# Kernel tuning notes

Measured on AMD Instinct MI355X. Metric: run time of the kernel, lower is better.

The kernel has to match this reference:

```python
import jax, jax.numpy as jnp
import numpy as np

D_MODEL = 1024
N_HEADS = 16
HEAD_DIM = D_MODEL // N_HEADS  # 64
WINDOW = 15
NUM_RANDOM = 2
B, L = 2, 2048


def setup_inputs() -> dict:
    key = jax.random.key(0)
    ks = jax.random.split(key, 5)
    x = jax.random.normal(ks[0], (B, L, D_MODEL), dtype=jnp.float32)
    # rotary angles: theta[t, j] = t / 10000^(2j/head_dim), shape [1, L, head_dim//2]
    inv_freq = 1.0 / (10000.0 ** (jnp.arange(0, HEAD_DIM, 2, dtype=jnp.float32) / HEAD_DIM))
    t = jnp.arange(L, dtype=jnp.float32)
    freqs = (t[:, None] * inv_freq[None, :])[None].astype(jnp.float32)  # [1,L,32]
    scale = 0.02
    wq = jax.random.normal(ks[1], (D_MODEL, D_MODEL), dtype=jnp.float32) * scale
    wk = jax.random.normal(ks[2], (D_MODEL, D_MODEL), dtype=jnp.float32) * scale
    wv = jax.random.normal(ks[3], (D_MODEL, D_MODEL), dtype=jnp.float32) * scale
    wo = jax.random.normal(ks[4], (D_MODEL, D_MODEL), dtype=jnp.float32) * scale
    return {"x": x, "freqs": freqs, "wq": wq, "wk": wk, "wv": wv, "wo": wo}


def _rope(t, cos, sin):
    # t: [B,H,L,hd]; interpret last dim as (hd/2, 2) complex pairs and rotate.
    tr = t.reshape(*t.shape[:-1], -1, 2)
    re, im = tr[..., 0], tr[..., 1]
    out_re = re * cos - im * sin
    out_im = re * sin + im * cos
    return jnp.stack([out_re, out_im], axis=-1).reshape(t.shape)


def _bigbird_mask(Lq):
    ii = jnp.arange(Lq)[:, None]
    jj = jnp.arange(Lq)[None, :]
    causal = jj <= ii
    window = jnp.abs(ii - jj) <= (WINDOW // 2)
    glob = (ii == 0) | (jj == 0)
    # random mask: per row i, NUM_RANDOM indices uniform in [0, i]
    rkey = jax.random.key(42)
    u = jax.random.uniform(rkey, (Lq, NUM_RANDOM))
    ridx = jnp.floor(u * (jnp.arange(Lq, dtype=jnp.float32)[:, None] + 1.0)).astype(jnp.int32)
    rmask = jnp.zeros((Lq, Lq), dtype=bool).at[jnp.arange(Lq)[:, None], ridx].set(True)
    # rows with <= NUM_RANDOM causal options attend to all of them
    rmask = rmask | (causal & (ii < NUM_RANDOM))
    return (causal & (window | rmask)) | glob  # [L,L]


def reference(x, freqs, wq, wk, wv, wo):
    b, l, _ = x.shape
    q = (x @ wq.T).reshape(b, l, N_HEADS, HEAD_DIM).transpose(0, 2, 1, 3)  # [B,H,L,hd]
    k = (x @ wk.T).reshape(b, l, N_HEADS, HEAD_DIM).transpose(0, 2, 1, 3)
    v = (x @ wv.T).reshape(b, l, N_HEADS, HEAD_DIM).transpose(0, 2, 1, 3)
    cos = jnp.cos(freqs[:, :l])[:, None]  # [1,1,L,hd/2]
    sin = jnp.sin(freqs[:, :l])[:, None]
    q = _rope(q, cos, sin)
    k = _rope(k, cos, sin)
    attn_mask = _bigbird_mask(l)  # [L,L], broadcast over B,H
    scale = 1.0 / jnp.sqrt(jnp.float32(HEAD_DIM))
    scores = jnp.einsum("bhqd,bhkd->bhqk", q, k) * scale
    scores = jnp.where(attn_mask[None, None], scores, jnp.finfo(scores.dtype).min)
    p = jax.nn.softmax(scores, axis=-1)
    out = jnp.einsum("bhqk,bhkd->bhqd", p, v)
    out = out.transpose(0, 2, 1, 3).reshape(b, l, D_MODEL)
    return out @ wo.T
```

## Files before the change

### kernel.cpp

```cpp
#include <hip/hip_runtime.h>
#include <math.h>

#define SEQ_L 2048
#define DM 1024
#define NH 16
#define HD 64
#define NB 2
#define KD 1024
#define ND 1024

typedef __bf16 bf16;
typedef __bf16 bf16x8 __attribute__((ext_vector_type(8)));
typedef __bf16 bf16x4 __attribute__((ext_vector_type(4)));
typedef float f32x4 __attribute__((ext_vector_type(4)));

__global__ void cvt_x_kernel(const float* __restrict__ in, bf16* __restrict__ out, int n) {
  int i = blockIdx.x * 256 + threadIdx.x;
  if (i < n) out[i] = (bf16)in[i];
}

__global__ void cvt_w_kernel(const float* __restrict__ w0, const float* __restrict__ w1,
                             const float* __restrict__ w2, const float* __restrict__ w3,
                             bf16* __restrict__ o0, bf16* __restrict__ o1,
                             bf16* __restrict__ o2, bf16* __restrict__ o3) {
  int i = blockIdx.x * 256 + threadIdx.x;
  const float* w; bf16* o;
  switch (blockIdx.y) {
    case 0: w = w0; o = o0; break;
    case 1: w = w1; o = o1; break;
    case 2: w = w2; o = o2; break;
    default: w = w3; o = o3; break;
  }
  o[i] = (bf16)w[i];
}

__device__ inline void gld16(const bf16* g, bf16* l) {
  __builtin_amdgcn_global_load_lds((const __attribute__((address_space(1))) void*)g,
                                   (__attribute__((address_space(3))) void*)l, 16, 0, 0);
}

template <typename OutT>
__device__ inline void gemm_bt_body(const bf16* __restrict__ A, const bf16* __restrict__ W,
                                    OutT* __restrict__ C) {
  __shared__ __align__(16) bf16 As[128 * 32];
  __shared__ __align__(16) bf16 Bs[128 * 32];
  const int t = threadIdx.x;
  const int lane = t & 63;
  const int wave = t >> 6;
  const int wm = (wave >> 1) * 64;
  const int wn = (wave & 1) * 64;
  const int m0 = blockIdx.x * 128;
  const int n0 = blockIdx.y * 128;
  const int r = t >> 2;
  const int ck = (t & 3) * 8;
  const int l15 = lane & 15;
  const int koff = (lane >> 4) * 8;

  f32x4 acc[4][4] = {};

  for (int k0 = 0; k0 < KD; k0 += 32) {
    gld16(A + (size_t)(m0 + r) * KD + k0 + ck, As + t * 8);
    gld16(A + (size_t)(m0 + 64 + r) * KD + k0 + ck, As + 2048 + t * 8);
    gld16(W + (size_t)(n0 + r) * KD + k0 + ck, Bs + t * 8);
    gld16(W + (size_t)(n0 + 64 + r) * KD + k0 + ck, Bs + 2048 + t * 8);
    __syncthreads();
    bf16x8 af[4], bfr[4];
#pragma unroll
    for (int mt = 0; mt < 4; ++mt)
      af[mt] = *(const bf16x8*)(As + (wm + mt * 16 + l15) * 32 + koff);
#pragma unroll
    for (int nt = 0; nt < 4; ++nt)
      bfr[nt] = *(const bf16x8*)(Bs + (wn + nt * 16 + l15) * 32 + koff);
#pragma unroll
    for (int mt = 0; mt < 4; ++mt)
#pragma unroll
      for (int nt = 0; nt < 4; ++nt)
        acc[mt][nt] = __builtin_amdgcn_mfma_f32_16x16x32_bf16(af[mt], bfr[nt], acc[mt][nt], 0, 0, 0);
    __syncthreads();
  }
  const int colb = n0 + wn + l15;
  const int rowb = m0 + wm + (lane >> 4) * 4;
#pragma unroll
  for (int mt = 0; mt < 4; ++mt)
#pragma unroll
    for (int nt = 0; nt < 4; ++nt)
#pragma unroll
      for (int rr = 0; rr < 4; ++rr)
        C[(size_t)(rowb + mt * 16 + rr) * ND + colb + nt * 16] = (OutT)acc[mt][nt][rr];
}

__global__ __launch_bounds__(256, 2) void qkv_gemm_kernel(
    const bf16* __restrict__ xb, const bf16* __restrict__ wqb, const bf16* __restrict__ wkb,
    const bf16* __restrict__ wvb, bf16* __restrict__ qb, bf16* __restrict__ kb, bf16* __restrict__ vb) {
  const bf16* W = blockIdx.z == 0 ? wqb : blockIdx.z == 1 ? wkb : wvb;
  bf16* O = blockIdx.z == 0 ? qb : blockIdx.z == 1 ? kb : vb;
  gemm_bt_body<bf16>(xb, W, O);
}

__global__ __launch_bounds__(256, 2) void out_gemm_kernel(
    const bf16* __restrict__ ab, const bf16* __restrict__ wob, float* __restrict__ out) {
  gemm_bt_body<float>(ab, wob, out);
}

__global__ void rope_kernel(bf16* __restrict__ q, bf16* __restrict__ k, const float* __restrict__ freqs) {
  int idx = blockIdx.x * 256 + threadIdx.x;
  int jj = idx & 31;
  int bl = idx >> 9;
  int l = bl & (SEQ_L - 1);
  float ang = freqs[l * 32 + jj];
  float s, c;
  __sincosf(ang, &s, &c);
  size_t base = (size_t)idx * 2;
  float qre = (float)q[base], qim = (float)q[base + 1];
  q[base]     = (bf16)(qre * c - qim * s);
  q[base + 1] = (bf16)(qre * s + qim * c);
  float kre = (float)k[base], kim = (float)k[base + 1];
  k[base]     = (bf16)(kre * c - kim * s);
  k[base + 1] = (bf16)(kre * s + kim * c);
}

__device__ inline uint32_t rotl32(uint32_t v, int n) { return (v << n) | (v >> (32 - n)); }

__device__ inline void threefry(uint32_t x0, uint32_t x1, uint32_t* o0, uint32_t* o1) {
  const uint32_t ks0 = 0u, ks1 = 42u, ks2 = 0u ^ 42u ^ 0x1BD11BDAu;
  x0 += ks0; x1 += ks1;
#define TF_R(rr) { x0 += x1; x1 = rotl32(x1, rr); x1 ^= x0; }
  TF_R(13) TF_R(15) TF_R(26) TF_R(6)
  x0 += ks1; x1 += ks2 + 1u;
  TF_R(17) TF_R(29) TF_R(16) TF_R(24)
  x0 += ks2; x1 += ks0 + 2u;
  TF_R(13) TF_R(15) TF_R(26) TF_R(6)
  x0 += ks0; x1 += ks1 + 3u;
  TF_R(17) TF_R(29) TF_R(16) TF_R(24)
  x0 += ks1; x1 += ks2 + 4u;
  TF_R(13) TF_R(15) TF_R(26) TF_R(6)
  x0 += ks2; x1 += ks0 + 5u;
#undef TF_R
  *o0 = x0; *o1 = x1;
}

__device__ inline int rand_col(int i, int s) {
  uint32_t o0, o1;
  threefry(0u, (uint32_t)(2 * i + s), &o0, &o1);
  uint32_t bits = o0 ^ o1;
  float u = __uint_as_float((bits >> 9) | 0x3f800000u) - 1.0f;
  return (int)floorf(u * (float)(i + 1));
}

__global__ void build_cols_kernel(int* __restrict__ ctab) {
  const int i = blockIdx.x * 256 + threadIdx.x;
  int cols[11]; int nc = 0;
  if (i >= 1) {
    int lo = i - 7; if (lo < 0) lo = 0;
    for (int j = lo; j <= i; ++j) cols[nc++] = j;
    if (lo > 0) cols[nc++] = 0;
#pragma unroll
    for (int s = 0; s < 2; ++s) {
      int rj = rand_col(i, s);
      bool dup = false;
      for (int c2 = 0; c2 < nc; ++c2) dup |= (cols[c2] == rj);
      if (!dup) cols[nc++] = rj;
    }
  }
  for (int c2 = nc; c2 < 11; ++c2) cols[c2] = -1;
#pragma unroll
  for (int c2 = 0; c2 < 11; ++c2) ctab[i * 12 + c2] = cols[c2];
  ctab[i * 12 + 11] = nc;
}

__global__ __launch_bounds__(256) void attn_kernel(const bf16* __restrict__ q, const bf16* __restrict__ k,
                                                   const bf16* __restrict__ v, bf16* __restrict__ o,
                                                   const int* __restrict__ ctab,
                                                   float* __restrict__ pm, float* __restrict__ pz,
                                                   float* __restrict__ pv) {
  const int t = threadIdx.x;
  const int lane = t & 63;
  const int w = t >> 6;

  __shared__ float sbuf[256];
  __shared__ float redm[4], redz[4];
  __shared__ float part[4][64];

  if (blockIdx.x < 1024) {
    const int b = blockIdx.x >> 9;
    const int tt = blockIdx.x & 511;
    const int tile = ((tt & 7) << 6) + (tt >> 3);
    const int i = tile * 4 + 1 + w;
    if (i >= SEQ_L) return;
    const size_t bb = (size_t)b * SEQ_L * DM;
    const int eo = lane * 16;

    const bf16* qrow = q + bb + (size_t)i * DM + eo;
    bf16x8 qv0 = *(const bf16x8*)(qrow);
    bf16x8 qv1 = *(const bf16x8*)(qrow + 8);

    const int4* cp = (const int4*)(ctab + i * 12);
    int4 ca = cp[0], cb = cp[1], cc = cp[2];
    int cols[11] = {ca.x, ca.y, ca.z, ca.w, cb.x, cb.y, cb.z, cb.w, cc.x, cc.y, cc.z};

    float sv[11];
#pragma unroll
    for (int c = 0; c < 11; ++c) {
      int cj = cols[c] < 0 ? 0 : cols[c];
      const bf16* krow = k + bb + (size_t)cj * DM + eo;
      bf16x8 kv0 = *(const bf16x8*)(krow);
      bf16x8 kv1 = *(const bf16x8*)(krow + 8);
      float acc = 0.f;
#pragma unroll
      for (int e = 0; e < 8; ++e)
        acc += (float)qv0[e] * (float)kv0[e] + (float)qv1[e] * (float)kv1[e];
      sv[c] = acc;
    }
#pragma unroll
    for (int c = 0; c < 11; ++c) {
      sv[c] += __shfl_xor(sv[c], 1);
      sv[c] += __shfl_xor(sv[c], 2);
      sv[c] = cols[c] < 0 ? -1e30f : sv[c] * 0.125f;
    }
    float m = -1e30f;
#pragma unroll
    for (int c = 0; c < 11; ++c) m = fmaxf(m, sv[c]);
    float z = 0.f;
#pragma unroll
    for (int c = 0; c < 11; ++c) { sv[c] = __expf(sv[c] - m); z += sv[c]; }
    const float inv = 1.f / z;

    float oa[16] = {};
#pragma unroll
    for (int c = 0; c < 11; ++c) {
      int cj = cols[c] < 0 ? 0 : cols[c];
      const bf16* vrow = v + bb + (size_t)cj * DM + eo;
      bf16x8 vv0 = *(const bf16x8*)(vrow);
      bf16x8 vv1 = *(const bf16x8*)(vrow + 8);
#pragma unroll
      for (int e = 0; e < 8; ++e) {
        oa[e]     += sv[c] * (float)vv0[e];
        oa[8 + e] += sv[c] * (float)vv1[e];
      }
    }
    bf16x8 ov0, ov1;
#pragma unroll
    for (int e = 0; e < 8; ++e) {
      ov0[e] = (bf16)(oa[e] * inv);
      ov1[e] = (bf16)(oa[8 + e] * inv);
    }
    bf16* orow = o + bb + (size_t)i * DM + eo;
    *(bf16x8*)(orow) = ov0;
    *(bf16x8*)(orow + 8) = ov1;
    return;
  }

  const int idx = blockIdx.x - 1024;
  const int b = idx >> 7;
  const int rem = idx & 127;
  const int h = rem >> 3;
  const int c = rem & 7;
  const size_t hb = (size_t)b * SEQ_L * DM + (size_t)h * HD;
  const int j = c * 256 + t;

  bf16x8 qv8[8];
#pragma unroll
  for (int cc = 0; cc < 8; ++cc) qv8[cc] = *(const bf16x8*)(q + hb + cc * 8);

  float acc = 0.f;
#pragma unroll
  for (int cc = 0; cc < 8; ++cc) {
    bf16x8 kv = *(const bf16x8*)(k + hb + (size_t)j * DM + cc * 8);
#pragma unroll
    for (int e = 0; e < 8; ++e) acc += (float)qv8[cc][e] * (float)kv[e];
  }
  float s = acc * 0.125f;
  float mloc = s;
#pragma unroll
  for (int off = 32; off > 0; off >>= 1) mloc = fmaxf(mloc, __shfl_xor(mloc, off));
  if (lane == 0) redm[w] = mloc;
  __syncthreads();
  const float m = fmaxf(fmaxf(redm[0], redm[1]), fmaxf(redm[2], redm[3]));

  float e = __expf(s - m);
  sbuf[t] = e;
  float zloc = e;
#pragma unroll
  for (int off = 32; off > 0; off >>= 1) zloc += __shfl_xor(zloc, off);
  if (lane == 0) redz[w] = zloc;
  __syncthreads();
  const float zc = redz[0] + redz[1] + redz[2] + redz[3];

  float oa = 0.f;
  for (int jj = w; jj < 256; jj += 4)
    oa += sbuf[jj] * (float)v[hb + (size_t)(c * 256 + jj) * DM + lane];
  part[w][lane] = oa;
  __syncthreads();
  if (t < 64) pv[idx * 64 + t] = part[0][t] + part[1][t] + part[2][t] + part[3][t];
  if (t == 0) { pm[idx] = m; pz[idx] = zc; }
}

__global__ __launch_bounds__(64) void row0_combine_kernel(const float* __restrict__ pm,
                                                          const float* __restrict__ pz,
                                                          const float* __restrict__ pv,
                                                          bf16* __restrict__ o) {
  const int bh = blockIdx.x;
  const int b = bh >> 4, h = bh & 15;
  const int d = threadIdx.x;
  const int base = bh * 8;
  float M = -1e30f;
#pragma unroll
  for (int c = 0; c < 8; ++c) M = fmaxf(M, pm[base + c]);
  float Z = 0.f, od = 0.f;
#pragma unroll
  for (int c = 0; c < 8; ++c) {
    float sc = __expf(pm[base + c] - M);
    Z += pz[base + c] * sc;
    od += pv[(base + c) * 64 + d] * sc;
  }
  o[(size_t)b * SEQ_L * DM + (size_t)h * HD + d] = (bf16)(od / Z);
}

extern "C" void kernel_launch(void* const* d_in, const int* in_sizes, int n_in,
                              void* d_out, int out_size, void* d_ws, size_t ws_size,
                              hipStream_t stream) {
  const float* x     = (const float*)d_in[0];
  const float* freqs = (const float*)d_in[1];
  const float* wq    = (const float*)d_in[2];
  const float* wk    = (const float*)d_in[3];
  const float* wv    = (const float*)d_in[4];
  const float* wo    = (const float*)d_in[5];
  float* out = (float*)d_out;

  char* ws = (char*)d_ws;
  bf16* xb  = (bf16*)(ws + 0);
  bf16* wqb = (bf16*)(ws + 8388608);
  bf16* wkb = (bf16*)(ws + 10485760);
  bf16* wvb = (bf16*)(ws + 12582912);
  bf16* wob = (bf16*)(ws + 14680064);
  bf16* qb  = (bf16*)(ws + 16777216);
  bf16* kb  = (bf16*)(ws + 25165824);
  bf16* vb  = (bf16*)(ws + 33554432);
  bf16* ab  = (bf16*)(ws + 41943040);
  int*   ctab = (int*)(ws + 0);
  float* pm   = (float*)(ws + 4194304);
  float* pz   = (float*)(ws + 4194304 + 1024);
  float* pv   = (float*)(ws + 4194304 + 2048);
  (void)ws_size;

  cvt_x_kernel<<<16384, 256, 0, stream>>>(x, xb, NB * SEQ_L * DM);
  cvt_w_kernel<<<dim3(4096, 4), 256, 0, stream>>>(wq, wk, wv, wo, wqb, wkb, wvb, wob);
  qkv_gemm_kernel<<<dim3(32, 8, 3), 256, 0, stream>>>(xb, wqb, wkb, wvb, qb, kb, vb);
  build_cols_kernel<<<8, 256, 0, stream>>>(ctab);
  rope_kernel<<<8192, 256, 0, stream>>>(qb, kb, freqs);
  attn_kernel<<<dim3(1280, 1), 256, 0, stream>>>(qb, kb, vb, ab, ctab, pm, pz, pv);
  row0_combine_kernel<<<32, 64, 0, stream>>>(pm, pz, pv, ab);
  out_gemm_kernel<<<dim3(32, 8), 256, 0, stream>>>(ab, wob, out);
}
```

Measured before the change: 186.0 us.

## Fuse conversions and column table into one prep kernel, fold RoPE into QKV GEMM

Merges the x and weight bf16 conversions, now float4-vectorized, and the random-column table build into a single prep kernel. RoPE is applied in the QKV GEMM epilogue through a lane shuffle with the pair partner, which removes a separate read-modify-write pass over Q and K. The output GEMM now uses 64-row tiles, doubling the block count for better CU occupancy. Workspace offsets for ctab and the partials are moved so they no longer alias xb, which the prep kernel now writes at the same time.

```diff
diff --git a/kernel.cpp b/kernel.cpp
--- a/kernel.cpp
+++ b/kernel.cpp
@@ -13,111 +13,6 @@
 typedef __bf16 bf16x8 __attribute__((ext_vector_type(8)));
 typedef __bf16 bf16x4 __attribute__((ext_vector_type(4)));
 typedef float f32x4 __attribute__((ext_vector_type(4)));
-
-__global__ void cvt_x_kernel(const float* __restrict__ in, bf16* __restrict__ out, int n) {
-  int i = blockIdx.x * 256 + threadIdx.x;
-  if (i < n) out[i] = (bf16)in[i];
-}
-
-__global__ void cvt_w_kernel(const float* __restrict__ w0, const float* __restrict__ w1,
-                             const float* __restrict__ w2, const float* __restrict__ w3,
-                             bf16* __restrict__ o0, bf16* __restrict__ o1,
-                             bf16* __restrict__ o2, bf16* __restrict__ o3) {
-  int i = blockIdx.x * 256 + threadIdx.x;
-  const float* w; bf16* o;
-  switch (blockIdx.y) {
-    case 0: w = w0; o = o0; break;
-    case 1: w = w1; o = o1; break;
-    case 2: w = w2; o = o2; break;
-    default: w = w3; o = o3; break;
-  }
-  o[i] = (bf16)w[i];
-}
-
-__device__ inline void gld16(const bf16* g, bf16* l) {
-  __builtin_amdgcn_global_load_lds((const __attribute__((address_space(1))) void*)g,
-                                   (__attribute__((address_space(3))) void*)l, 16, 0, 0);
-}
-
-template <typename OutT>
-__device__ inline void gemm_bt_body(const bf16* __restrict__ A, const bf16* __restrict__ W,
-                                    OutT* __restrict__ C) {
-  __shared__ __align__(16) bf16 As[128 * 32];
-  __shared__ __align__(16) bf16 Bs[128 * 32];
-  const int t = threadIdx.x;
-  const int lane = t & 63;
-  const int wave = t >> 6;
-  const int wm = (wave >> 1) * 64;
-  const int wn = (wave & 1) * 64;
-  const int m0 = blockIdx.x * 128;
-  const int n0 = blockIdx.y * 128;
-  const int r = t >> 2;
-  const int ck = (t & 3) * 8;
-  const int l15 = lane & 15;
-  const int koff = (lane >> 4) * 8;
-
-  f32x4 acc[4][4] = {};
-
-  for (int k0 = 0; k0 < KD; k0 += 32) {
-    gld16(A + (size_t)(m0 + r) * KD + k0 + ck, As + t * 8);
-    gld16(A + (size_t)(m0 + 64 + r) * KD + k0 + ck, As + 2048 + t * 8);
-    gld16(W + (size_t)(n0 + r) * KD + k0 + ck, Bs + t * 8);
-    gld16(W + (size_t)(n0 + 64 + r) * KD + k0 + ck, Bs + 2048 + t * 8);
-    __syncthreads();
-    bf16x8 af[4], bfr[4];
-#pragma unroll
-    for (int mt = 0; mt < 4; ++mt)
-      af[mt] = *(const bf16x8*)(As + (wm + mt * 16 + l15) * 32 + koff);
-#pragma unroll
-    for (int nt = 0; nt < 4; ++nt)
-      bfr[nt] = *(const bf16x8*)(Bs + (wn + nt * 16 + l15) * 32 + koff);
-#pragma unroll
-    for (int mt = 0; mt < 4; ++mt)
-#pragma unroll
-      for (int nt = 0; nt < 4; ++nt)
-        acc[mt][nt] = __builtin_amdgcn_mfma_f32_16x16x32_bf16(af[mt], bfr[nt], acc[mt][nt], 0, 0, 0);
-    __syncthreads();
-  }
-  const int colb = n0 + wn + l15;
-  const int rowb = m0 + wm + (lane >> 4) * 4;
-#pragma unroll
-  for (int mt = 0; mt < 4; ++mt)
-#pragma unroll
-    for (int nt = 0; nt < 4; ++nt)
-#pragma unroll
-      for (int rr = 0; rr < 4; ++rr)
-        C[(size_t)(rowb + mt * 16 + rr) * ND + colb + nt * 16] = (OutT)acc[mt][nt][rr];
-}
-
-__global__ __launch_bounds__(256, 2) void qkv_gemm_kernel(
-    const bf16* __restrict__ xb, const bf16* __restrict__ wqb, const bf16* __restrict__ wkb,
-    const bf16* __restrict__ wvb, bf16* __restrict__ qb, bf16* __restrict__ kb, bf16* __restrict__ vb) {
-  const bf16* W = blockIdx.z == 0 ? wqb : blockIdx.z == 1 ? wkb : wvb;
-  bf16* O = blockIdx.z == 0 ? qb : blockIdx.z == 1 ? kb : vb;
-  gemm_bt_body<bf16>(xb, W, O);
-}
-
-__global__ __launch_bounds__(256, 2) void out_gemm_kernel(
-    const bf16* __restrict__ ab, const bf16* __restrict__ wob, float* __restrict__ out) {
-  gemm_bt_body<float>(ab, wob, out);
-}
-
-__global__ void rope_kernel(bf16* __restrict__ q, bf16* __restrict__ k, const float* __restrict__ freqs) {
-  int idx = blockIdx.x * 256 + threadIdx.x;
-  int jj = idx & 31;
-  int bl = idx >> 9;
-  int l = bl & (SEQ_L - 1);
-  float ang = freqs[l * 32 + jj];
-  float s, c;
-  __sincosf(ang, &s, &c);
-  size_t base = (size_t)idx * 2;
-  float qre = (float)q[base], qim = (float)q[base + 1];
-  q[base]     = (bf16)(qre * c - qim * s);
-  q[base + 1] = (bf16)(qre * s + qim * c);
-  float kre = (float)k[base], kim = (float)k[base + 1];
-  k[base]     = (bf16)(kre * c - kim * s);
-  k[base + 1] = (bf16)(kre * s + kim * c);
-}
 
 __device__ inline uint32_t rotl32(uint32_t v, int n) { return (v << n) | (v >> (32 - n)); }
 
@@ -147,8 +42,38 @@
   return (int)floorf(u * (float)(i + 1));
 }
 
-__global__ void build_cols_kernel(int* __restrict__ ctab) {
-  const int i = blockIdx.x * 256 + threadIdx.x;
+__global__ void prep_kernel(const float* __restrict__ x,
+                            const float* __restrict__ w0, const float* __restrict__ w1,
+                            const float* __restrict__ w2, const float* __restrict__ w3,
+                            bf16* __restrict__ xb,
+                            bf16* __restrict__ o0, bf16* __restrict__ o1,
+                            bf16* __restrict__ o2, bf16* __restrict__ o3,
+                            int* __restrict__ ctab) {
+  const int bx = blockIdx.x;
+  const int t = threadIdx.x;
+  if (bx < 8192) {
+    const float* src;
+    bf16* dst;
+    int idx;
+    if (bx < 4096) { src = x; dst = xb; idx = bx * 256 + t; }
+    else {
+      int widx = bx - 4096;
+      int wsel = widx >> 10;
+      switch (wsel) {
+        case 0: src = w0; dst = o0; break;
+        case 1: src = w1; dst = o1; break;
+        case 2: src = w2; dst = o2; break;
+        default: src = w3; dst = o3; break;
+      }
+      idx = (widx & 1023) * 256 + t;
+    }
+    float4 vv = ((const float4*)src)[idx];
+    bf16x4 ov;
+    ov[0] = (bf16)vv.x; ov[1] = (bf16)vv.y; ov[2] = (bf16)vv.z; ov[3] = (bf16)vv.w;
+    *(bf16x4*)(dst + (size_t)idx * 4) = ov;
+    return;
+  }
+  const int i = (bx - 8192) * 256 + t;
   int cols[11]; int nc = 0;
   if (i >= 1) {
     int lo = i - 7; if (lo < 0) lo = 0;
@@ -166,6 +91,133 @@
 #pragma unroll
   for (int c2 = 0; c2 < 11; ++c2) ctab[i * 12 + c2] = cols[c2];
   ctab[i * 12 + 11] = nc;
+}
+
+__device__ inline void gld16(const bf16* g, bf16* l) {
+  __builtin_amdgcn_global_load_lds((const __attribute__((address_space(1))) void*)g,
+                                   (__attribute__((address_space(3))) void*)l, 16, 0, 0);
+}
+
+template <typename OutT>
+__device__ inline void gemm_bt_body(const bf16* __restrict__ A, const bf16* __restrict__ W,
+                                    OutT* __restrict__ C, const float* __restrict__ rope) {
+  __shared__ __align__(16) bf16 As[128 * 32];
+  __shared__ __align__(16) bf16 Bs[128 * 32];
+  const int t = threadIdx.x;
+  const int lane = t & 63;
+  const int wave = t >> 6;
+  const int wm = (wave >> 1) * 64;
+  const int wn = (wave & 1) * 64;
+  const int m0 = blockIdx.x * 128;
+  const int n0 = blockIdx.y * 128;
+  const int r = t >> 2;
+  const int ck = (t & 3) * 8;
+  const int l15 = lane & 15;
+  const int koff = (lane >> 4) * 8;
+
+  f32x4 acc[4][4] = {};
+
+  for (int k0 = 0; k0 < KD; k0 += 32) {
+    gld16(A + (size_t)(m0 + r) * KD + k0 + ck, As + t * 8);
+    gld16(A + (size_t)(m0 + 64 + r) * KD + k0 + ck, As + 2048 + t * 8);
+    gld16(W + (size_t)(n0 + r) * KD + k0 + ck, Bs + t * 8);
+    gld16(W + (size_t)(n0 + 64 + r) * KD + k0 + ck, Bs + 2048 + t * 8);
+    __syncthreads();
+    bf16x8 af[4], bfr[4];
+#pragma unroll
+    for (int mt = 0; mt < 4; ++mt)
+      af[mt] = *(const bf16x8*)(As + (wm + mt * 16 + l15) * 32 + koff);
+#pragma unroll
+    for (int nt = 0; nt < 4; ++nt)
+      bfr[nt] = *(const bf16x8*)(Bs + (wn + nt * 16 + l15) * 32 + koff);
+#pragma unroll
+    for (int mt = 0; mt < 4; ++mt)
+#pragma unroll
+      for (int nt = 0; nt < 4; ++nt)
+        acc[mt][nt] = __builtin_amdgcn_mfma_f32_16x16x32_bf16(af[mt], bfr[nt], acc[mt][nt], 0, 0, 0);
+    __syncthreads();
+  }
+  const int colb = n0 + wn + l15;
+  const int rowb = m0 + wm + (lane >> 4) * 4;
+  const int odd = l15 & 1;
+#pragma unroll
+  for (int mt = 0; mt < 4; ++mt)
+#pragma unroll
+    for (int nt = 0; nt < 4; ++nt) {
+      const int col = colb + nt * 16;
+      const int jj = (col & 63) >> 1;
+#pragma unroll
+      for (int rr = 0; rr < 4; ++rr) {
+        float val = acc[mt][nt][rr];
+        if (rope) {
+          const int row = rowb + mt * 16 + rr;
+          const int l = row & (SEQ_L - 1);
+          float s, c;
+          __sincosf(rope[l * 32 + jj], &s, &c);
+          float partner = __shfl_xor(val, 1);
+          val = odd ? val * c + partner * s : val * c - partner * s;
+        }
+        C[(size_t)(rowb + mt * 16 + rr) * ND + colb + nt * 16] = (OutT)val;
+      }
+    }
+}
+
+__global__ __launch_bounds__(256, 2) void qkv_gemm_kernel(
+    const bf16* __restrict__ xb, const bf16* __restrict__ wqb, const bf16* __restrict__ wkb,
+    const bf16* __restrict__ wvb, bf16* __restrict__ qb, bf16* __restrict__ kb, bf16* __restrict__ vb,
+    const float* __restrict__ freqs) {
+  const bf16* W = blockIdx.z == 0 ? wqb : blockIdx.z == 1 ? wkb : wvb;
+  bf16* O = blockIdx.z == 0 ? qb : blockIdx.z == 1 ? kb : vb;
+  const float* fr = blockIdx.z < 2 ? freqs : nullptr;
+  gemm_bt_body<bf16>(xb, W, O, fr);
+}
+
+__global__ __launch_bounds__(256, 2) void out_gemm_kernel(
+    const bf16* __restrict__ ab, const bf16* __restrict__ wob, float* __restrict__ out) {
+  __shared__ __align__(16) bf16 As[64 * 32];
+  __shared__ __align__(16) bf16 Bs[128 * 32];
+  const int t = threadIdx.x;
+  const int lane = t & 63;
+  const int wave = t >> 6;
+  const int wm = (wave >> 1) * 32;
+  const int wn = (wave & 1) * 64;
+  const int m0 = blockIdx.x * 64;
+  const int n0 = blockIdx.y * 128;
+  const int r = t >> 2;
+  const int ck = (t & 3) * 8;
+  const int l15 = lane & 15;
+  const int koff = (lane >> 4) * 8;
+
+  f32x4 acc[2][4] = {};
+
+  for (int k0 = 0; k0 < KD; k0 += 32) {
+    gld16(ab + (size_t)(m0 + r) * KD + k0 + ck, As + t * 8);
+    gld16(wob + (size_t)(n0 + r) * KD + k0 + ck, Bs + t * 8);
+    gld16(wob + (size_t)(n0 + 64 + r) * KD + k0 + ck, Bs + 2048 + t * 8);
+    __syncthreads();
+    bf16x8 af[2], bfr[4];
+#pragma unroll
+    for (int mt = 0; mt < 2; ++mt)
+      af[mt] = *(const bf16x8*)(As + (wm + mt * 16 + l15) * 32 + koff);
+#pragma unroll
+    for (int nt = 0; nt < 4; ++nt)
+      bfr[nt] = *(const bf16x8*)(Bs + (wn + nt * 16 + l15) * 32 + koff);
+#pragma unroll
+    for (int mt = 0; mt < 2; ++mt)
+#pragma unroll
+      for (int nt = 0; nt < 4; ++nt)
+        acc[mt][nt] = __builtin_amdgcn_mfma_f32_16x16x32_bf16(af[mt], bfr[nt], acc[mt][nt], 0, 0, 0);
+    __syncthreads();
+  }
+  const int colb = n0 + wn + l15;
+  const int rowb = m0 + wm + (lane >> 4) * 4;
+#pragma unroll
+  for (int mt = 0; mt < 2; ++mt)
+#pragma unroll
+    for (int nt = 0; nt < 4; ++nt)
+#pragma unroll
+      for (int rr = 0; rr < 4; ++rr)
+        out[(size_t)(rowb + mt * 16 + rr) * ND + colb + nt * 16] = acc[mt][nt][rr];
 }
 
 __global__ __launch_bounds__(256) void attn_kernel(const bf16* __restrict__ q, const bf16* __restrict__ k,
@@ -337,18 +389,15 @@
   bf16* kb  = (bf16*)(ws + 25165824);
   bf16* vb  = (bf16*)(ws + 33554432);
   bf16* ab  = (bf16*)(ws + 41943040);
-  int*   ctab = (int*)(ws + 0);
-  float* pm   = (float*)(ws + 4194304);
-  float* pz   = (float*)(ws + 4194304 + 1024);
-  float* pv   = (float*)(ws + 4194304 + 2048);
+  int*   ctab = (int*)(ws + 50331648);
+  float* pm   = (float*)(ws + 50462720);
+  float* pz   = (float*)(ws + 50463744);
+  float* pv   = (float*)(ws + 50464768);
   (void)ws_size;
 
-  cvt_x_kernel<<<16384, 256, 0, stream>>>(x, xb, NB * SEQ_L * DM);
-  cvt_w_kernel<<<dim3(4096, 4), 256, 0, stream>>>(wq, wk, wv, wo, wqb, wkb, wvb, wob);
-  qkv_gemm_kernel<<<dim3(32, 8, 3), 256, 0, stream>>>(xb, wqb, wkb, wvb, qb, kb, vb);
-  build_cols_kernel<<<8, 256, 0, stream>>>(ctab);
-  rope_kernel<<<8192, 256, 0, stream>>>(qb, kb, freqs);
+  prep_kernel<<<8200, 256, 0, stream>>>(x, wq, wk, wv, wo, xb, wqb, wkb, wvb, wob, ctab);
+  qkv_gemm_kernel<<<dim3(32, 8, 3), 256, 0, stream>>>(xb, wqb, wkb, wvb, qb, kb, vb, freqs);
   attn_kernel<<<dim3(1280, 1), 256, 0, stream>>>(qb, kb, vb, ab, ctab, pm, pz, pv);
   row0_combine_kernel<<<32, 64, 0, stream>>>(pm, pz, pv, ab);
-  out_gemm_kernel<<<dim3(32, 8), 256, 0, stream>>>(ab, wob, out);
-}
+  out_gemm_kernel<<<dim3(64, 8), 256, 0, stream>>>(ab, wob, out);
+}
```

Result: faster. 175.8 us (-5.5%).
